# Kernel optimization log

Hardware: AMD Instinct MI355X
Metric: run time of the kernel (lower is better)

Reference implementation:

```python
import jax, jax.numpy as jnp
import numpy as np

INPUT_DIM = 512
LATENT_DIM = 64
H1, H2 = 128, 64  # hardcoded hidden widths in Encoder/Decoder
BATCH = 4096


def _xavier(key, shape):
    fan_out, fan_in = shape
    std = jnp.sqrt(2.0 / (fan_in + fan_out))
    return std * jax.random.normal(key, shape, dtype=jnp.float32)


def setup_inputs() -> dict:
    key = jax.random.key(0)
    ks = jax.random.split(key, 10)
    d = LATENT_DIM
    n_pairs = d * (d - 1) // 2
    n_funcs = 1 + d + n_pairs  # bias + states + pairwise products
    inp = {
        "x": jax.random.normal(ks[0], (BATCH, INPUT_DIM), dtype=jnp.float32),
        "xdot": jax.random.normal(ks[1], (BATCH, INPUT_DIM), dtype=jnp.float32),
        # encoder weights (torch Linear layout: [out, in])
        "We1": _xavier(ks[2], (H1, INPUT_DIM)), "be1": jnp.zeros((H1,), jnp.float32),
        "We2": _xavier(ks[3], (H2, H1)),        "be2": jnp.zeros((H2,), jnp.float32),
        "We3": _xavier(ks[4], (d, H2)),         "be3": jnp.zeros((d,), jnp.float32),
        # decoder weights
        "Wd1": _xavier(ks[5], (H2, d)),         "bd1": jnp.zeros((H2,), jnp.float32),
        "Wd2": _xavier(ks[6], (H1, H2)),        "bd2": jnp.zeros((H1,), jnp.float32),
        "Wd3": _xavier(ks[7], (INPUT_DIM, H1)), "bd3": jnp.zeros((INPUT_DIM,), jnp.float32),
        "XI": jnp.ones((n_funcs, d), jnp.float32),
        "XI_mask": jnp.ones((n_funcs, d), jnp.float32),
    }
    return inp


def _mlp_with_jacobian(x, Ws, bs):
    """3-layer relu MLP; returns output and per-sample analytic Jacobian [B,out,in].
    Jacobian = diag(m3) W3 diag(m2) W2 diag(m1) W1 with relu masks m_l."""
    h = x
    J = None
    for W, b in zip(Ws, bs):
        h = h @ W.T + b                      # [B, out_l]
        m = (h > 0).astype(h.dtype)          # relu mask (grad 0 at 0, matching torch)
        h = jnp.maximum(h, 0)
        Wm = m[:, :, None] * W[None]         # [B, out_l, in_l]
        J = Wm if J is None else jnp.einsum('boh,bhi->boi', Wm, J)
    return h, J


def _sindy_library(z):
    B, d = z.shape
    iu, ju = np.triu_indices(d, k=1)
    ones = jnp.ones((B, 1), z.dtype)
    pairs = z[:, iu] * z[:, ju]              # [B, d(d-1)/2]
    return jnp.concatenate([ones, z, pairs], axis=1)


def reference(x, xdot, We1, be1, We2, be2, We3, be3,
              Wd1, bd1, Wd2, bd2, Wd3, bd3, XI, XI_mask):
    z, Jenc = _mlp_with_jacobian(x, (We1, We2, We3), (be1, be2, be3))
    dz_dt = jnp.einsum('bli,bi->bl', Jenc, xdot)
    xh, Jdec = _mlp_with_jacobian(z, (Wd1, Wd2, Wd3), (bd1, bd2, bd3))
    theta = _sindy_library(z)
    dz_dt_sindy = theta @ (XI_mask * XI)
    dxh_dt = jnp.einsum('bol,bl->bo', Jdec, dz_dt_sindy)
    return (xh, dxh_dt, z, dz_dt, dz_dt_sindy)
```

## Files before the change

### kernel.cpp

```cpp
#include <hip/hip_runtime.h>

#define BATCH 4096
#define IN_DIM 512
#define H1DIM 128
#define H2DIM 64
#define DDIM 64
#define NFUNC 2081
#define NFPAD 2112
#define CHUNK 704
#define KS_PER_CHUNK 22

typedef short bf16x8 __attribute__((ext_vector_type(8)));
typedef float f32x4 __attribute__((ext_vector_type(4)));
#define MFMA(a,b,c) __builtin_amdgcn_mfma_f32_16x16x32_bf16(a,b,c,0,0,0)

#define WSZ1 (H1DIM*IN_DIM)
#define WSZ2 (H2DIM*H1DIM)
#define WSZ3 (DDIM*H2DIM)
#define WSZ4 (H2DIM*DDIM)
#define WSZ5 (H1DIM*H2DIM)
#define WSZ6 (IN_DIM*H1DIM)

__device__ __forceinline__ short f2b(float f) {
    union { float f; unsigned u; } x; x.f = f;
    unsigned r = x.u + 0x7fffu + ((x.u >> 16) & 1u);
    return (short)(r >> 16);
}
__device__ __forceinline__ float b2f(short s) {
    union { unsigned u; float f; } x; x.u = ((unsigned)(unsigned short)s) << 16;
    return x.f;
}
__device__ __forceinline__ void split3f(float v, short& s0, short& s1, short& s2) {
    s0 = f2b(v); float r = v - b2f(s0);
    s1 = f2b(r); float r2 = r - b2f(s1);
    s2 = f2b(r2);
}
__device__ __forceinline__ uint2 pk4(const short* s) {
    union { short s[4]; uint2 u; } z;
    z.s[0] = s[0]; z.s[1] = s[1]; z.s[2] = s[2]; z.s[3] = s[3];
    return z.u;
}

__device__ __forceinline__ void st_b16(short* t, int RS, int r, int c, short v) {
    int b = (c * 2) ^ ((r & 7) << 4);
    *(short*)((char*)(t + r * RS) + b) = v;
}
__device__ __forceinline__ void st_b64(short* t, int RS, int r, int c0, uint2 v) {
    int b = (c0 * 2) ^ ((r & 7) << 4);
    *(uint2*)((char*)(t + r * RS) + b) = v;
}
__device__ __forceinline__ bf16x8 ld_af(const short* t, int RS, int lane, int kbase) {
    int r = lane & 15;
    int b = ((kbase + (lane >> 4) * 8) * 2) ^ ((r & 7) << 4);
    return *(const bf16x8*)((const char*)(t + r * RS) + b);
}
__device__ __forceinline__ bf16x8 ld_bp(const short* P, int blk, int lane) {
    return *(const bf16x8*)(P + ((size_t)blk * 64 + lane) * 8);
}

__device__ __forceinline__ void mf9(bf16x8 f0, bf16x8 f1, bf16x8 f2, bf16x8 fv,
                                    bf16x8 b0, bf16x8 b1, bf16x8 b2,
                                    f32x4& P, f32x4& Q, f32x4& V) {
    P = MFMA(f0, b0, P); Q = MFMA(f1, b1, Q);
    P = MFMA(f1, b0, P); Q = MFMA(f0, b1, Q);
    P = MFMA(f2, b0, P); Q = MFMA(f2, b1, Q);
    P = MFMA(f0, b2, P); Q = MFMA(f1, b2, Q);
    V = MFMA(fv, b0, V);
}

__device__ __forceinline__ void epi_store(short* t0, short* t1, short* t2, short* tv, int RS,
                                          int lane, int col, const f32x4& P, const f32x4& Q,
                                          const f32x4& V, float bb)
{
    #pragma unroll
    for (int q = 0; q < 4; ++q) {
        int row = (lane >> 4) * 4 + q;
        float pre = P[q] + Q[q] + bb;
        float h = fmaxf(pre, 0.f);
        short s0, s1, s2;
        split3f(h, s0, s1, s2);
        st_b16(t0, RS, row, col, s0);
        st_b16(t1, RS, row, col, s1);
        st_b16(t2, RS, row, col, s2);
        st_b16(tv, RS, row, col, pre > 0.f ? f2b(V[q]) : (short)0);
    }
}

template<int K>
__device__ void pack_w(const float* __restrict__ W, short* __restrict__ dst, int NK,
                       int gid, int nthr)
{
    for (int i = gid; i < NK; i += nthr) {
        int c = i / K, k = i % K;
        int cb = c >> 4, ks = k >> 5;
        int L = (((k >> 3) & 3) << 4) | (c & 15);
        int j = k & 7;
        int idx = ((cb * (K / 32) + ks) * 64 + L) * 8 + j;
        short s0, s1, s2; split3f(W[i], s0, s1, s2);
        dst[idx] = s0; dst[idx + NK] = s1; dst[idx + 2 * NK] = s2;
    }
}

__global__ void initk(const float* __restrict__ x, const float* __restrict__ xdot,
                      const float* __restrict__ We1, const float* __restrict__ We2,
                      const float* __restrict__ We3, const float* __restrict__ Wd1,
                      const float* __restrict__ Wd2, const float* __restrict__ Wd3,
                      const float* __restrict__ XI, const float* __restrict__ XIm,
                      float* __restrict__ xh, float* __restrict__ dxh,
                      short* Wp1, short* Wp2, short* Wp3, short* Wp4, short* Wp5, short* Wp6,
                      short* xiP, int2* pk)
{
    int gid = blockIdx.x * blockDim.x + threadIdx.x;
    int nthr = gridDim.x * blockDim.x;

    for (int i = gid; i < (BATCH / 16) * 16 * 64; i += nthr) {
        int L = i & 63, ks = (i >> 6) & 15, rb = i >> 10;
        int row = rb * 16 + (L & 15);
        int k0 = ks * 32 + ((L >> 4) << 3);
        const float* px = &x[(size_t)row * IN_DIM + k0];
        const float* pd = &xdot[(size_t)row * IN_DIM + k0];
        union { short s[8]; bf16x8 v; } a0, a1, a2, dv;
        #pragma unroll
        for (int j = 0; j < 8; ++j) {
            split3f(px[j], a0.s[j], a1.s[j], a2.s[j]);
            dv.s[j] = f2b(pd[j]);
        }
        short* bx = (short*)(xh + (size_t)rb * 8192);
        short* bd = (short*)(dxh + (size_t)rb * 8192);
        int off = (ks * 64 + L) * 8;
        *(bf16x8*)(bx + off) = a0.v;
        *(bf16x8*)(bx + 8192 + off) = a1.v;
        *(bf16x8*)(bd + off) = a2.v;
        *(bf16x8*)(bd + 8192 + off) = dv.v;
    }

    pack_w<512>(We1, Wp1, WSZ1, gid, nthr);
    pack_w<128>(We2, Wp2, WSZ2, gid, nthr);
    pack_w<64>(We3, Wp3, WSZ3, gid, nthr);
    pack_w<64>(Wd1, Wp4, WSZ4, gid, nthr);
    pack_w<64>(Wd2, Wp5, WSZ5, gid, nthr);
    pack_w<128>(Wd3, Wp6, WSZ6, gid, nthr);

    for (int i = gid; i < 4 * 66 * 64; i += nthr) {
        int cb = i / (66 * 64);
        int r = i - cb * (66 * 64);
        int ks = r >> 6, L = r & 63;
        int col = cb * 16 + (L & 15);
        union { short s[8]; bf16x8 v; } w;
        #pragma unroll
        for (int j = 0; j < 8; ++j) {
            int f = ks * 32 + ((L >> 4) << 3) + j;
            float v = (f < NFUNC) ? XI[(size_t)f * DDIM + col] * XIm[(size_t)f * DDIM + col] : 0.f;
            w.s[j] = f2b(v);
        }
        *(bf16x8*)(xiP + (size_t)i * 8) = w.v;
    }

    for (int f = gid; f < NFPAD; f += nthr) {
        int a, b;
        if (f == 0) { a = 64; b = 64; }
        else if (f <= DDIM) { a = f - 1; b = 64; }
        else if (f < NFUNC) {
            int p = f - 1 - DDIM; int i2 = 0, cum = 0;
            while (cum + (63 - i2) <= p) { cum += 63 - i2; ++i2; }
            a = i2; b = i2 + 1 + (p - cum);
        } else { a = 65; b = 65; }
        pk[f] = make_int2(a, b);
    }
}

__global__ __launch_bounds__(256, 1)
void fused(const float* __restrict__ be1, const float* __restrict__ be2,
           const float* __restrict__ be3, const float* __restrict__ bd1,
           const float* __restrict__ bd2, const float* __restrict__ bd3,
           const short* __restrict__ Wp1, const short* __restrict__ Wp2,
           const short* __restrict__ Wp3, const short* __restrict__ Wp4,
           const short* __restrict__ Wp5, const short* __restrict__ Wp6,
           const short* __restrict__ xiP, const int2* __restrict__ pk,
           float* __restrict__ xh, float* __restrict__ dxh, float* __restrict__ zo,
           float* __restrict__ dz, float* __restrict__ dzs)
{
    __shared__ __align__(16) char ldsbuf[37120];
    short* h1s0 = (short*)(ldsbuf + 0);
    short* h1s1 = (short*)(ldsbuf + 4096);
    short* h1s2 = (short*)(ldsbuf + 8192);
    short* v1   = (short*)(ldsbuf + 12288);
    short* h2s0 = (short*)(ldsbuf + 16384);
    short* h2s1 = (short*)(ldsbuf + 18432);
    short* h2s2 = (short*)(ldsbuf + 20480);
    short* v2   = (short*)(ldsbuf + 22528);
    short* th   = (short*)(ldsbuf + 0);
    short* g1s0 = (short*)(ldsbuf + 0);
    short* g1s1 = (short*)(ldsbuf + 2048);
    short* g1s2 = (short*)(ldsbuf + 4096);
    short* u1   = (short*)(ldsbuf + 6144);
    short* g2s0 = (short*)(ldsbuf + 8192);
    short* g2s1 = (short*)(ldsbuf + 12288);
    short* g2s2 = (short*)(ldsbuf + 16384);
    short* u2   = (short*)(ldsbuf + 20480);
    short* zb0  = (short*)(ldsbuf + 24576);
    short* zb1  = (short*)(ldsbuf + 26624);
    short* zb2  = (short*)(ldsbuf + 28672);
    short* dzsb = (short*)(ldsbuf + 30720);
    float* zf   = (float*)(ldsbuf + 32768);

    const int tid = threadIdx.x, lane = tid & 63, wave = tid >> 6;
    const int row0 = blockIdx.x * 16;
    const int c16 = lane & 15;

    float bb1[2] = { be1[wave * 32 + c16], be1[wave * 32 + 16 + c16] };
    float bb2 = be2[wave * 16 + c16];
    float bb3 = be3[wave * 16 + c16];
    float bD1 = bd1[wave * 16 + c16];
    float bD2[2] = { bd2[wave * 32 + c16], bd2[wave * 32 + 16 + c16] };
    float bD3[8];
    #pragma unroll
    for (int i = 0; i < 8; ++i) bD3[i] = bd3[wave * 128 + i * 16 + c16];

    bf16x8 L2B[4][3];

    {
        const short* bx = (const short*)(xh + (size_t)blockIdx.x * 8192);
        const short* bd = (const short*)(dxh + (size_t)blockIdx.x * 8192);
        f32x4 P[2] = {}, Q[2] = {}, V[2] = {};
        bf16x8 A0[3], A1[3], A2[3], Ad[3];
        bf16x8 B0[3][2], B1[3][2], B2[3][2];
#define L1_LA(ks, sl) { int off = ((ks) * 64 + lane) * 8; \
        A0[sl] = *(const bf16x8*)(bx + off); A1[sl] = *(const bf16x8*)(bx + 8192 + off); \
        A2[sl] = *(const bf16x8*)(bd + off); Ad[sl] = *(const bf16x8*)(bd + 8192 + off); }
#define L1_LB(ks, sl) { int bA = (wave * 2) * 16 + (ks), bB = (wave * 2 + 1) * 16 + (ks); \
        B0[sl][0] = ld_bp(Wp1, bA, lane); B1[sl][0] = ld_bp(Wp1 + WSZ1, bA, lane); B2[sl][0] = ld_bp(Wp1 + 2 * WSZ1, bA, lane); \
        B0[sl][1] = ld_bp(Wp1, bB, lane); B1[sl][1] = ld_bp(Wp1 + WSZ1, bB, lane); B2[sl][1] = ld_bp(Wp1 + 2 * WSZ1, bB, lane); }
        L1_LA(0, 0) L1_LB(0, 0)
        L1_LA(1, 1) L1_LB(1, 1)
        L1_LA(2, 2) L1_LB(2, 2)
        #pragma unroll
        for (int ks = 0; ks < 16; ++ks) {
            const int sl = ks % 3;
            mf9(A0[sl], A1[sl], A2[sl], Ad[sl], B0[sl][0], B1[sl][0], B2[sl][0], P[0], Q[0], V[0]);
            mf9(A0[sl], A1[sl], A2[sl], Ad[sl], B0[sl][1], B1[sl][1], B2[sl][1], P[1], Q[1], V[1]);
            if (ks + 3 < 16) { L1_LA(ks + 3, sl) L1_LB(ks + 3, sl) }
        }
#undef L1_LA
#undef L1_LB
        #pragma unroll
        for (int nf = 0; nf < 2; ++nf) {
            int col = wave * 32 + nf * 16 + c16;
            epi_store(h1s0, h1s1, h1s2, v1, 128, lane, col, P[nf], Q[nf], V[nf], bb1[nf]);
        }
        #pragma unroll
        for (int ks = 0; ks < 4; ++ks) {
            int blk = wave * 4 + ks;
            L2B[ks][0] = ld_bp(Wp2, blk, lane);
            L2B[ks][1] = ld_bp(Wp2 + WSZ2, blk, lane);
            L2B[ks][2] = ld_bp(Wp2 + 2 * WSZ2, blk, lane);
        }
    }
    __syncthreads();

    bf16x8 L3B[2][3];
    {
        bf16x8 Aa[4][4];
        #pragma unroll
        for (int ks = 0; ks < 4; ++ks) {
            Aa[ks][0] = ld_af(h1s0, 128, lane, ks * 32);
            Aa[ks][1] = ld_af(h1s1, 128, lane, ks * 32);
            Aa[ks][2] = ld_af(h1s2, 128, lane, ks * 32);
            Aa[ks][3] = ld_af(v1, 128, lane, ks * 32);
        }
        f32x4 P = {}, Q = {}, V = {};
        #pragma unroll
        for (int ks = 0; ks < 4; ++ks)
            mf9(Aa[ks][0], Aa[ks][1], Aa[ks][2], Aa[ks][3], L2B[ks][0], L2B[ks][1], L2B[ks][2], P, Q, V);
        epi_store(h2s0, h2s1, h2s2, v2, 64, lane, wave * 16 + c16, P, Q, V, bb2);
        #pragma unroll
        for (int ks = 0; ks < 2; ++ks) {
            int blk = wave * 2 + ks;
            L3B[ks][0] = ld_bp(Wp3, blk, lane);
            L3B[ks][1] = ld_bp(Wp3 + WSZ3, blk, lane);
            L3B[ks][2] = ld_bp(Wp3 + 2 * WSZ3, blk, lane);
        }
    }
    __syncthreads();

    {
        bf16x8 Aa[2][4];
        #pragma unroll
        for (int ks = 0; ks < 2; ++ks) {
            Aa[ks][0] = ld_af(h2s0, 64, lane, ks * 32);
            Aa[ks][1] = ld_af(h2s1, 64, lane, ks * 32);
            Aa[ks][2] = ld_af(h2s2, 64, lane, ks * 32);
            Aa[ks][3] = ld_af(v2, 64, lane, ks * 32);
        }
        f32x4 P = {}, Q = {}, V = {};
        #pragma unroll
        for (int ks = 0; ks < 2; ++ks)
            mf9(Aa[ks][0], Aa[ks][1], Aa[ks][2], Aa[ks][3], L3B[ks][0], L3B[ks][1], L3B[ks][2], P, Q, V);
        int col = wave * 16 + c16;
        #pragma unroll
        for (int q = 0; q < 4; ++q) {
            int row = (lane >> 4) * 4 + q;
            float pre = P[q] + Q[q] + bb3;
            float hz = fmaxf(pre, 0.f);
            float vz = pre > 0.f ? V[q] : 0.f;
            zf[row * 68 + col] = hz;
            short s0, s1, s2;
            split3f(hz, s0, s1, s2);
            st_b16(zb0, 64, row, col, s0);
            st_b16(zb1, 64, row, col, s1);
            st_b16(zb2, 64, row, col, s2);
            zo[(size_t)(row0 + row) * DDIM + col] = hz;
            dz[(size_t)(row0 + row) * DDIM + col] = vz;
        }
        if (tid < 32) { int r = tid & 15; zf[r * 68 + 64 + (tid >> 4)] = (tid >> 4) ? 0.f : 1.f; }
    }
    __syncthreads();

    {
        f32x4 sa0 = {}, sa1 = {};
        const int tr = tid & 15, tf44 = (tid >> 4) * 44;
        bf16x8 X[KS_PER_CHUNK];
        #pragma unroll
        for (int kk = 0; kk < KS_PER_CHUNK; ++kk)
            X[kk] = ld_bp(xiP, wave * 66 + kk, lane);
        #pragma unroll
        for (int ch = 0; ch < 3; ++ch) {
            #pragma unroll
            for (int g = 0; g < 11; ++g) {
                int fl = tf44 + g * 4;
                int fg = ch * CHUNK + fl;
                int4 qa = *(const int4*)&pk[fg];
                int4 qb = *(const int4*)&pk[fg + 2];
                float t0 = zf[tr * 68 + qa.x] * zf[tr * 68 + qa.y];
                float t1 = zf[tr * 68 + qa.z] * zf[tr * 68 + qa.w];
                float t2 = zf[tr * 68 + qb.x] * zf[tr * 68 + qb.y];
                float t3 = zf[tr * 68 + qb.z] * zf[tr * 68 + qb.w];
                short arr[4] = { f2b(t0), f2b(t1), f2b(t2), f2b(t3) };
                st_b64(th, 704, tr, fl, pk4(arr));
            }
            __syncthreads();
            #pragma unroll
            for (int kk = 0; kk < KS_PER_CHUNK; ++kk) {
                bf16x8 a = ld_af(th, 704, lane, kk * 32);
                if (kk & 1) sa1 = MFMA(a, X[kk], sa1);
                else        sa0 = MFMA(a, X[kk], sa0);
            }
            if (ch < 2) {
                #pragma unroll
                for (int kk = 0; kk < KS_PER_CHUNK; ++kk)
                    X[kk] = ld_bp(xiP, wave * 66 + (ch + 1) * KS_PER_CHUNK + kk, lane);
            }
            __syncthreads();
        }
        f32x4 sacc = sa0 + sa1;
        int col = wave * 16 + c16;
        #pragma unroll
        for (int q = 0; q < 4; ++q) {
            int row = (lane >> 4) * 4 + q;
            float v = sacc[q];
            dzs[(size_t)(row0 + row) * DDIM + col] = v;
            st_b16(dzsb, 64, row, col, f2b(v));
        }
    }
    bf16x8 D1B[2][3];
    #pragma unroll
    for (int ks = 0; ks < 2; ++ks) {
        int blk = wave * 2 + ks;
        D1B[ks][0] = ld_bp(Wp4, blk, lane);
        D1B[ks][1] = ld_bp(Wp4 + WSZ4, blk, lane);
        D1B[ks][2] = ld_bp(Wp4 + 2 * WSZ4, blk, lane);
    }
    __syncthreads();

    bf16x8 D2B[2][2][3];
    {
        bf16x8 Aa[2][4];
        #pragma unroll
        for (int ks = 0; ks < 2; ++ks) {
            Aa[ks][0] = ld_af(zb0, 64, lane, ks * 32);
            Aa[ks][1] = ld_af(zb1, 64, lane, ks * 32);
            Aa[ks][2] = ld_af(zb2, 64, lane, ks * 32);
            Aa[ks][3] = ld_af(dzsb, 64, lane, ks * 32);
        }
        f32x4 P = {}, Q = {}, V = {};
        #pragma unroll
        for (int ks = 0; ks < 2; ++ks)
            mf9(Aa[ks][0], Aa[ks][1], Aa[ks][2], Aa[ks][3], D1B[ks][0], D1B[ks][1], D1B[ks][2], P, Q, V);
        epi_store(g1s0, g1s1, g1s2, u1, 64, lane, wave * 16 + c16, P, Q, V, bD1);
        #pragma unroll
        for (int cf = 0; cf < 2; ++cf)
            #pragma unroll
            for (int ks = 0; ks < 2; ++ks) {
                int blk = (wave * 2 + cf) * 2 + ks;
                D2B[cf][ks][0] = ld_bp(Wp5, blk, lane);
                D2B[cf][ks][1] = ld_bp(Wp5 + WSZ5, blk, lane);
                D2B[cf][ks][2] = ld_bp(Wp5 + 2 * WSZ5, blk, lane);
            }
    }
    __syncthreads();

    {
        bf16x8 Aa[2][4];
        #pragma unroll
        for (int ks = 0; ks < 2; ++ks) {
            Aa[ks][0] = ld_af(g1s0, 64, lane, ks * 32);
            Aa[ks][1] = ld_af(g1s1, 64, lane, ks * 32);
            Aa[ks][2] = ld_af(g1s2, 64, lane, ks * 32);
            Aa[ks][3] = ld_af(u1, 64, lane, ks * 32);
        }
        f32x4 P[2] = {}, Q[2] = {}, V[2] = {};
        #pragma unroll
        for (int cf = 0; cf < 2; ++cf)
            #pragma unroll
            for (int ks = 0; ks < 2; ++ks)
                mf9(Aa[ks][0], Aa[ks][1], Aa[ks][2], Aa[ks][3],
                    D2B[cf][ks][0], D2B[cf][ks][1], D2B[cf][ks][2], P[cf], Q[cf], V[cf]);
        #pragma unroll
        for (int cf = 0; cf < 2; ++cf) {
            int col = wave * 32 + cf * 16 + c16;
            epi_store(g2s0, g2s1, g2s2, u2, 128, lane, col, P[cf], Q[cf], V[cf], bD2[cf]);
        }
    }
    __syncthreads();

    #pragma unroll
    for (int h = 0; h < 2; ++h) {
        f32x4 P[4] = {}, Q[4] = {}, V[4] = {};
        bf16x8 Bp[4][3];
        bf16x8 Ax0[2], Ax1[2], Ax2[2], Axv[2];
#define D3_LA(ks, b) { Ax0[b] = ld_af(g2s0, 128, lane, (ks) * 32); Ax1[b] = ld_af(g2s1, 128, lane, (ks) * 32); \
                       Ax2[b] = ld_af(g2s2, 128, lane, (ks) * 32); Axv[b] = ld_af(u2, 128, lane, (ks) * 32); }
#define D3_LB(s, sl) { int blk = (wave * 8 + h * 4 + ((s) & 3)) * 4 + ((s) >> 2); \
        Bp[sl][0] = ld_bp(Wp6, blk, lane); Bp[sl][1] = ld_bp(Wp6 + WSZ6, blk, lane); Bp[sl][2] = ld_bp(Wp6 + 2 * WSZ6, blk, lane); }
        D3_LA(0, 0)
        D3_LB(0, 0) D3_LB(1, 1) D3_LB(2, 2) D3_LB(3, 3)
        #pragma unroll
        for (int ks = 0; ks < 4; ++ks) {
            if (ks < 3) D3_LA(ks + 1, (ks + 1) & 1)
            #pragma unroll
            for (int cf = 0; cf < 4; ++cf) {
                const int s = ks * 4 + cf, sl = s & 3;
                mf9(Ax0[ks & 1], Ax1[ks & 1], Ax2[ks & 1], Axv[ks & 1],
                    Bp[sl][0], Bp[sl][1], Bp[sl][2], P[cf], Q[cf], V[cf]);
                if (s + 4 < 16) D3_LB(s + 4, sl)
            }
        }
#undef D3_LA
#undef D3_LB
        #pragma unroll
        for (int cf = 0; cf < 4; ++cf) {
            int col = wave * 128 + h * 64 + cf * 16 + c16;
            float bb = bD3[h * 4 + cf];
            #pragma unroll
            for (int q = 0; q < 4; ++q) {
                int row = (lane >> 4) * 4 + q;
                float pre = P[cf][q] + Q[cf][q] + bb;
                xh[(size_t)(row0 + row) * IN_DIM + col] = fmaxf(pre, 0.f);
                dxh[(size_t)(row0 + row) * IN_DIM + col] = pre > 0.f ? V[cf][q] : 0.f;
            }
        }
    }
}

extern "C" void kernel_launch(void* const* d_in, const int* in_sizes, int n_in,
                              void* d_out, int out_size, void* d_ws, size_t ws_size,
                              hipStream_t stream)
{
    const float* x    = (const float*)d_in[0];
    const float* xdot = (const float*)d_in[1];
    const float* We1  = (const float*)d_in[2];
    const float* be1  = (const float*)d_in[3];
    const float* We2  = (const float*)d_in[4];
    const float* be2  = (const float*)d_in[5];
    const float* We3  = (const float*)d_in[6];
    const float* be3  = (const float*)d_in[7];
    const float* Wd1  = (const float*)d_in[8];
    const float* bd1  = (const float*)d_in[9];
    const float* Wd2  = (const float*)d_in[10];
    const float* bd2  = (const float*)d_in[11];
    const float* Wd3  = (const float*)d_in[12];
    const float* bd3  = (const float*)d_in[13];
    const float* XI   = (const float*)d_in[14];
    const float* XIm  = (const float*)d_in[15];

    float* out = (float*)d_out;
    float* xh  = out;
    float* dxh = out + (size_t)BATCH * IN_DIM;
    float* zo  = dxh + (size_t)BATCH * IN_DIM;
    float* dz  = zo + (size_t)BATCH * DDIM;
    float* dzs = dz + (size_t)BATCH * DDIM;

    int2*  pk  = (int2*)d_ws;
    short* Wp1 = (short*)(pk + NFPAD);
    short* Wp2 = Wp1 + 3 * WSZ1;
    short* Wp3 = Wp2 + 3 * WSZ2;
    short* Wp4 = Wp3 + 3 * WSZ3;
    short* Wp5 = Wp4 + 3 * WSZ4;
    short* Wp6 = Wp5 + 3 * WSZ5;
    short* xiP = Wp6 + 3 * WSZ6;

    initk<<<1024, 256, 0, stream>>>(x, xdot, We1, We2, We3, Wd1, Wd2, Wd3, XI, XIm,
                                    xh, dxh, Wp1, Wp2, Wp3, Wp4, Wp5, Wp6, xiP, pk);
    fused<<<BATCH / 16, 256, 0, stream>>>(be1, be2, be3, bd1, bd2, bd3,
                                          Wp1, Wp2, Wp3, Wp4, Wp5, Wp6, xiP, pk,
                                          xh, dxh, zo, dz, dzs);
}
```

Before: 51.31 us.

## Stream layer-1 and decoder-3 operands through LDS with async global_load_lds pipeline

Replaces the register-prefetched global loads in the first encoder GEMM and the last decoder GEMM with asynchronous global-to-LDS copies (global_load_lds) into per-wave multi-slot ring buffers. Explicit vmcnt waits and sched barriers control how far the loads run ahead. Several weight prefetches (Wp2, Wp3, XI, Wp4, Wp5) are also moved earlier so they overlap preceding MFMA work. LDS grows to 120KB, which keeps occupancy at one block per CU, and the hand-tuned waitcnt values are fragile if the instruction count changes.

```diff
diff --git a/kernel.cpp b/kernel.cpp
--- a/kernel.cpp
+++ b/kernel.cpp
@@ -39,6 +39,11 @@
     union { short s[4]; uint2 u; } z;
     z.s[0] = s[0]; z.s[1] = s[1]; z.s[2] = s[2]; z.s[3] = s[3];
     return z.u;
+}
+
+template<int N> __device__ __forceinline__ void waitv() {
+    asm volatile("s_waitcnt vmcnt(%0)" :: "n"(N) : "memory");
+    __builtin_amdgcn_sched_barrier(0);
 }
 
 __device__ __forceinline__ void st_b16(short* t, int RS, int r, int c, short v) {
@@ -180,33 +185,39 @@
            float* __restrict__ xh, float* __restrict__ dxh, float* __restrict__ zo,
            float* __restrict__ dz, float* __restrict__ dzs)
 {
-    __shared__ __align__(16) char ldsbuf[37120];
-    short* h1s0 = (short*)(ldsbuf + 0);
-    short* h1s1 = (short*)(ldsbuf + 4096);
-    short* h1s2 = (short*)(ldsbuf + 8192);
-    short* v1   = (short*)(ldsbuf + 12288);
-    short* h2s0 = (short*)(ldsbuf + 16384);
-    short* h2s1 = (short*)(ldsbuf + 18432);
-    short* h2s2 = (short*)(ldsbuf + 20480);
-    short* v2   = (short*)(ldsbuf + 22528);
-    short* th   = (short*)(ldsbuf + 0);
-    short* g1s0 = (short*)(ldsbuf + 0);
-    short* g1s1 = (short*)(ldsbuf + 2048);
-    short* g1s2 = (short*)(ldsbuf + 4096);
-    short* u1   = (short*)(ldsbuf + 6144);
-    short* g2s0 = (short*)(ldsbuf + 8192);
-    short* g2s1 = (short*)(ldsbuf + 12288);
-    short* g2s2 = (short*)(ldsbuf + 16384);
-    short* u2   = (short*)(ldsbuf + 20480);
-    short* zb0  = (short*)(ldsbuf + 24576);
-    short* zb1  = (short*)(ldsbuf + 26624);
-    short* zb2  = (short*)(ldsbuf + 28672);
-    short* dzsb = (short*)(ldsbuf + 30720);
-    float* zf   = (float*)(ldsbuf + 32768);
+    __shared__ __align__(1024) char lds[122880];
+#define GLL(gp, lo) __builtin_amdgcn_global_load_lds( \
+        (const __attribute__((address_space(1))) unsigned int*)(gp), \
+        (__attribute__((address_space(3))) unsigned int*)&lds[lo], 16, 0, 0)
+
+    short* h1s0 = (short*)(lds + 0);
+    short* h1s1 = (short*)(lds + 4096);
+    short* h1s2 = (short*)(lds + 8192);
+    short* v1   = (short*)(lds + 12288);
+    short* h2s0 = (short*)(lds + 16384);
+    short* h2s1 = (short*)(lds + 18432);
+    short* h2s2 = (short*)(lds + 20480);
+    short* v2   = (short*)(lds + 22528);
+    short* th   = (short*)(lds + 0);
+    short* g1s0 = (short*)(lds + 0);
+    short* g1s1 = (short*)(lds + 2048);
+    short* g1s2 = (short*)(lds + 4096);
+    short* u1   = (short*)(lds + 6144);
+    short* g2s0 = (short*)(lds + 8192);
+    short* g2s1 = (short*)(lds + 12288);
+    short* g2s2 = (short*)(lds + 16384);
+    short* u2   = (short*)(lds + 20480);
+    short* zb0  = (short*)(lds + 24576);
+    short* zb1  = (short*)(lds + 26624);
+    short* zb2  = (short*)(lds + 28672);
+    short* dzsb = (short*)(lds + 30720);
+    float* zf   = (float*)(lds + 32768);
 
     const int tid = threadIdx.x, lane = tid & 63, wave = tid >> 6;
     const int row0 = blockIdx.x * 16;
     const int c16 = lane & 15;
+    const int lane16 = lane * 16;
+    const int tr = tid & 15, tf44 = (tid >> 4) * 44;
 
     float bb1[2] = { be1[wave * 32 + c16], be1[wave * 32 + 16 + c16] };
     float bb2 = be2[wave * 16 + c16];
@@ -217,44 +228,61 @@
     #pragma unroll
     for (int i = 0; i < 8; ++i) bD3[i] = bd3[wave * 128 + i * 16 + c16];
 
+    f32x4 P1[2] = {}, Q1[2] = {}, V1[2] = {};
+    {
+        const char* bxc = (const char*)(xh + (size_t)blockIdx.x * 8192);
+        const char* bdc = (const char*)(dxh + (size_t)blockIdx.x * 8192);
+        const char* w1ac = (const char*)Wp1;
+        const char* w1bc = (const char*)(Wp1 + WSZ1);
+        const char* w1cc = (const char*)(Wp1 + 2 * WSZ1);
+#define SLOT1(d) (unsigned)(wave * 30720 + (d) * 10240)
+#define ISS1(ks, d) { unsigned sb = SLOT1(d); \
+        const char* ga = bxc + (ks) * 1024 + lane16; \
+        GLL(ga, sb);            GLL(ga + 16384, sb + 1024); \
+        const char* gd = bdc + (ks) * 1024 + lane16; \
+        GLL(gd, sb + 2048);     GLL(gd + 16384, sb + 3072); \
+        int bA = ((wave * 2) * 16 + (ks)) * 1024 + lane16; \
+        int bB = ((wave * 2 + 1) * 16 + (ks)) * 1024 + lane16; \
+        GLL(w1ac + bA, sb + 4096); GLL(w1bc + bA, sb + 5120); GLL(w1cc + bA, sb + 6144); \
+        GLL(w1ac + bB, sb + 7168); GLL(w1bc + bB, sb + 8192); GLL(w1cc + bB, sb + 9216); }
+#define STEP1(ks, WN) { waitv<WN>(); unsigned sb = SLOT1((ks) % 3); \
+        bf16x8 f0  = *(const bf16x8*)&lds[sb + lane16]; \
+        bf16x8 f1  = *(const bf16x8*)&lds[sb + 1024 + lane16]; \
+        bf16x8 f2  = *(const bf16x8*)&lds[sb + 2048 + lane16]; \
+        bf16x8 fv  = *(const bf16x8*)&lds[sb + 3072 + lane16]; \
+        bf16x8 b00 = *(const bf16x8*)&lds[sb + 4096 + lane16]; \
+        bf16x8 b01 = *(const bf16x8*)&lds[sb + 5120 + lane16]; \
+        bf16x8 b02 = *(const bf16x8*)&lds[sb + 6144 + lane16]; \
+        bf16x8 b10 = *(const bf16x8*)&lds[sb + 7168 + lane16]; \
+        bf16x8 b11 = *(const bf16x8*)&lds[sb + 8192 + lane16]; \
+        bf16x8 b12 = *(const bf16x8*)&lds[sb + 9216 + lane16]; \
+        mf9(f0, f1, f2, fv, b00, b01, b02, P1[0], Q1[0], V1[0]); \
+        mf9(f0, f1, f2, fv, b10, b11, b12, P1[1], Q1[1], V1[1]); \
+        __builtin_amdgcn_sched_barrier(0); \
+        if ((ks) + 3 < 16) ISS1((ks) + 3, (ks) % 3) }
+
+        ISS1(0, 0) ISS1(1, 1) ISS1(2, 2)
+        STEP1(0, 20)  STEP1(1, 20)  STEP1(2, 20)  STEP1(3, 20)
+        STEP1(4, 20)  STEP1(5, 20)  STEP1(6, 20)  STEP1(7, 20)
+        STEP1(8, 20)  STEP1(9, 20)  STEP1(10, 20) STEP1(11, 20)
+        STEP1(12, 20) STEP1(13, 20) STEP1(14, 10) STEP1(15, 0)
+#undef ISS1
+#undef STEP1
+#undef SLOT1
+    }
+    __syncthreads();
+    #pragma unroll
+    for (int nf = 0; nf < 2; ++nf) {
+        int col = wave * 32 + nf * 16 + c16;
+        epi_store(h1s0, h1s1, h1s2, v1, 128, lane, col, P1[nf], Q1[nf], V1[nf], bb1[nf]);
+    }
     bf16x8 L2B[4][3];
-
-    {
-        const short* bx = (const short*)(xh + (size_t)blockIdx.x * 8192);
-        const short* bd = (const short*)(dxh + (size_t)blockIdx.x * 8192);
-        f32x4 P[2] = {}, Q[2] = {}, V[2] = {};
-        bf16x8 A0[3], A1[3], A2[3], Ad[3];
-        bf16x8 B0[3][2], B1[3][2], B2[3][2];
-#define L1_LA(ks, sl) { int off = ((ks) * 64 + lane) * 8; \
-        A0[sl] = *(const bf16x8*)(bx + off); A1[sl] = *(const bf16x8*)(bx + 8192 + off); \
-        A2[sl] = *(const bf16x8*)(bd + off); Ad[sl] = *(const bf16x8*)(bd + 8192 + off); }
-#define L1_LB(ks, sl) { int bA = (wave * 2) * 16 + (ks), bB = (wave * 2 + 1) * 16 + (ks); \
-        B0[sl][0] = ld_bp(Wp1, bA, lane); B1[sl][0] = ld_bp(Wp1 + WSZ1, bA, lane); B2[sl][0] = ld_bp(Wp1 + 2 * WSZ1, bA, lane); \
-        B0[sl][1] = ld_bp(Wp1, bB, lane); B1[sl][1] = ld_bp(Wp1 + WSZ1, bB, lane); B2[sl][1] = ld_bp(Wp1 + 2 * WSZ1, bB, lane); }
-        L1_LA(0, 0) L1_LB(0, 0)
-        L1_LA(1, 1) L1_LB(1, 1)
-        L1_LA(2, 2) L1_LB(2, 2)
-        #pragma unroll
-        for (int ks = 0; ks < 16; ++ks) {
-            const int sl = ks % 3;
-            mf9(A0[sl], A1[sl], A2[sl], Ad[sl], B0[sl][0], B1[sl][0], B2[sl][0], P[0], Q[0], V[0]);
-            mf9(A0[sl], A1[sl], A2[sl], Ad[sl], B0[sl][1], B1[sl][1], B2[sl][1], P[1], Q[1], V[1]);
-            if (ks + 3 < 16) { L1_LA(ks + 3, sl) L1_LB(ks + 3, sl) }
-        }
-#undef L1_LA
-#undef L1_LB
-        #pragma unroll
-        for (int nf = 0; nf < 2; ++nf) {
-            int col = wave * 32 + nf * 16 + c16;
-            epi_store(h1s0, h1s1, h1s2, v1, 128, lane, col, P[nf], Q[nf], V[nf], bb1[nf]);
-        }
-        #pragma unroll
-        for (int ks = 0; ks < 4; ++ks) {
-            int blk = wave * 4 + ks;
-            L2B[ks][0] = ld_bp(Wp2, blk, lane);
-            L2B[ks][1] = ld_bp(Wp2 + WSZ2, blk, lane);
-            L2B[ks][2] = ld_bp(Wp2 + 2 * WSZ2, blk, lane);
-        }
+    #pragma unroll
+    for (int ks = 0; ks < 4; ++ks) {
+        int blk = wave * 4 + ks;
+        L2B[ks][0] = ld_bp(Wp2, blk, lane);
+        L2B[ks][1] = ld_bp(Wp2 + WSZ2, blk, lane);
+        L2B[ks][2] = ld_bp(Wp2 + 2 * WSZ2, blk, lane);
     }
     __syncthreads();
 
@@ -268,11 +296,6 @@
             Aa[ks][2] = ld_af(h1s2, 128, lane, ks * 32);
             Aa[ks][3] = ld_af(v1, 128, lane, ks * 32);
         }
-        f32x4 P = {}, Q = {}, V = {};
-        #pragma unroll
-        for (int ks = 0; ks < 4; ++ks)
-            mf9(Aa[ks][0], Aa[ks][1], Aa[ks][2], Aa[ks][3], L2B[ks][0], L2B[ks][1], L2B[ks][2], P, Q, V);
-        epi_store(h2s0, h2s1, h2s2, v2, 64, lane, wave * 16 + c16, P, Q, V, bb2);
         #pragma unroll
         for (int ks = 0; ks < 2; ++ks) {
             int blk = wave * 2 + ks;
@@ -280,9 +303,15 @@
             L3B[ks][1] = ld_bp(Wp3 + WSZ3, blk, lane);
             L3B[ks][2] = ld_bp(Wp3 + 2 * WSZ3, blk, lane);
         }
-    }
-    __syncthreads();
-
+        f32x4 P = {}, Q = {}, V = {};
+        #pragma unroll
+        for (int ks = 0; ks < 4; ++ks)
+            mf9(Aa[ks][0], Aa[ks][1], Aa[ks][2], Aa[ks][3], L2B[ks][0], L2B[ks][1], L2B[ks][2], P, Q, V);
+        epi_store(h2s0, h2s1, h2s2, v2, 64, lane, wave * 16 + c16, P, Q, V, bb2);
+    }
+    __syncthreads();
+
+    bf16x8 X[KS_PER_CHUNK];
     {
         bf16x8 Aa[2][4];
         #pragma unroll
@@ -296,6 +325,9 @@
         #pragma unroll
         for (int ks = 0; ks < 2; ++ks)
             mf9(Aa[ks][0], Aa[ks][1], Aa[ks][2], Aa[ks][3], L3B[ks][0], L3B[ks][1], L3B[ks][2], P, Q, V);
+        #pragma unroll
+        for (int kk = 0; kk < KS_PER_CHUNK; ++kk)
+            X[kk] = ld_bp(xiP, wave * 66 + kk, lane);
         int col = wave * 16 + c16;
         #pragma unroll
         for (int q = 0; q < 4; ++q) {
@@ -316,43 +348,46 @@
     }
     __syncthreads();
 
-    {
-        f32x4 sa0 = {}, sa1 = {};
-        const int tr = tid & 15, tf44 = (tid >> 4) * 44;
-        bf16x8 X[KS_PER_CHUNK];
-        #pragma unroll
-        for (int kk = 0; kk < KS_PER_CHUNK; ++kk)
-            X[kk] = ld_bp(xiP, wave * 66 + kk, lane);
-        #pragma unroll
-        for (int ch = 0; ch < 3; ++ch) {
-            #pragma unroll
-            for (int g = 0; g < 11; ++g) {
-                int fl = tf44 + g * 4;
-                int fg = ch * CHUNK + fl;
-                int4 qa = *(const int4*)&pk[fg];
-                int4 qb = *(const int4*)&pk[fg + 2];
-                float t0 = zf[tr * 68 + qa.x] * zf[tr * 68 + qa.y];
-                float t1 = zf[tr * 68 + qa.z] * zf[tr * 68 + qa.w];
-                float t2 = zf[tr * 68 + qb.x] * zf[tr * 68 + qb.y];
-                float t3 = zf[tr * 68 + qb.z] * zf[tr * 68 + qb.w];
-                short arr[4] = { f2b(t0), f2b(t1), f2b(t2), f2b(t3) };
-                st_b64(th, 704, tr, fl, pk4(arr));
-            }
-            __syncthreads();
-            #pragma unroll
-            for (int kk = 0; kk < KS_PER_CHUNK; ++kk) {
-                bf16x8 a = ld_af(th, 704, lane, kk * 32);
-                if (kk & 1) sa1 = MFMA(a, X[kk], sa1);
-                else        sa0 = MFMA(a, X[kk], sa0);
-            }
-            if (ch < 2) {
-                #pragma unroll
-                for (int kk = 0; kk < KS_PER_CHUNK; ++kk)
-                    X[kk] = ld_bp(xiP, wave * 66 + (ch + 1) * KS_PER_CHUNK + kk, lane);
-            }
-            __syncthreads();
-        }
+    f32x4 sa0 = {}, sa1 = {};
+#define BUILD(ch) { _Pragma("unroll") for (int g = 0; g < 11; ++g) { \
+        int fl = tf44 + g * 4, fg = (ch) * CHUNK + fl; \
+        int4 qa = *(const int4*)&pk[fg]; int4 qb = *(const int4*)&pk[fg + 2]; \
+        float t0 = zf[tr * 68 + qa.x] * zf[tr * 68 + qa.y]; \
+        float t1 = zf[tr * 68 + qa.z] * zf[tr * 68 + qa.w]; \
+        float t2 = zf[tr * 68 + qb.x] * zf[tr * 68 + qb.y]; \
+        float t3 = zf[tr * 68 + qb.z] * zf[tr * 68 + qb.w]; \
+        short arr[4] = { f2b(t0), f2b(t1), f2b(t2), f2b(t3) }; \
+        st_b64(th, 704, tr, fl, pk4(arr)); } }
+#define SMF() { _Pragma("unroll") for (int kk = 0; kk < KS_PER_CHUNK; ++kk) { \
+        bf16x8 a = ld_af(th, 704, lane, kk * 32); \
+        if (kk & 1) sa1 = MFMA(a, X[kk], sa1); else sa0 = MFMA(a, X[kk], sa0); } }
+#define ISX(ch) { _Pragma("unroll") for (int kk = 0; kk < KS_PER_CHUNK; ++kk) \
+        X[kk] = ld_bp(xiP, wave * 66 + (ch) * KS_PER_CHUNK + kk, lane); }
+
+    BUILD(0)
+    __syncthreads();
+    SMF() ISX(1)
+    __syncthreads();
+    BUILD(1)
+    __syncthreads();
+    SMF() ISX(2)
+    __syncthreads();
+    BUILD(2)
+    __syncthreads();
+    SMF()
+#undef BUILD
+#undef SMF
+#undef ISX
+    bf16x8 D1B[2][3];
+    {
         f32x4 sacc = sa0 + sa1;
+        #pragma unroll
+        for (int ks = 0; ks < 2; ++ks) {
+            int blk = wave * 2 + ks;
+            D1B[ks][0] = ld_bp(Wp4, blk, lane);
+            D1B[ks][1] = ld_bp(Wp4 + WSZ4, blk, lane);
+            D1B[ks][2] = ld_bp(Wp4 + 2 * WSZ4, blk, lane);
+        }
         int col = wave * 16 + c16;
         #pragma unroll
         for (int q = 0; q < 4; ++q) {
@@ -362,17 +397,9 @@
             st_b16(dzsb, 64, row, col, f2b(v));
         }
     }
-    bf16x8 D1B[2][3];
-    #pragma unroll
-    for (int ks = 0; ks < 2; ++ks) {
-        int blk = wave * 2 + ks;
-        D1B[ks][0] = ld_bp(Wp4, blk, lane);
-        D1B[ks][1] = ld_bp(Wp4 + WSZ4, blk, lane);
-        D1B[ks][2] = ld_bp(Wp4 + 2 * WSZ4, blk, lane);
-    }
-    __syncthreads();
-
-    bf16x8 D2B[2][2][3];
+    __syncthreads();
+
+    bf16x8 D2B[4][3];
     {
         bf16x8 Aa[2][4];
         #pragma unroll
@@ -382,20 +409,20 @@
             Aa[ks][2] = ld_af(zb2, 64, lane, ks * 32);
             Aa[ks][3] = ld_af(dzsb, 64, lane, ks * 32);
         }
-        f32x4 P = {}, Q = {}, V = {};
-        #pragma unroll
-        for (int ks = 0; ks < 2; ++ks)
-            mf9(Aa[ks][0], Aa[ks][1], Aa[ks][2], Aa[ks][3], D1B[ks][0], D1B[ks][1], D1B[ks][2], P, Q, V);
-        epi_store(g1s0, g1s1, g1s2, u1, 64, lane, wave * 16 + c16, P, Q, V, bD1);
         #pragma unroll
         for (int cf = 0; cf < 2; ++cf)
             #pragma unroll
             for (int ks = 0; ks < 2; ++ks) {
                 int blk = (wave * 2 + cf) * 2 + ks;
-                D2B[cf][ks][0] = ld_bp(Wp5, blk, lane);
-                D2B[cf][ks][1] = ld_bp(Wp5 + WSZ5, blk, lane);
-                D2B[cf][ks][2] = ld_bp(Wp5 + 2 * WSZ5, blk, lane);
+                D2B[cf * 2 + ks][0] = ld_bp(Wp5, blk, lane);
+                D2B[cf * 2 + ks][1] = ld_bp(Wp5 + WSZ5, blk, lane);
+                D2B[cf * 2 + ks][2] = ld_bp(Wp5 + 2 * WSZ5, blk, lane);
             }
+        f32x4 P = {}, Q = {}, V = {};
+        #pragma unroll
+        for (int ks = 0; ks < 2; ++ks)
+            mf9(Aa[ks][0], Aa[ks][1], Aa[ks][2], Aa[ks][3], D1B[ks][0], D1B[ks][1], D1B[ks][2], P, Q, V);
+        epi_store(g1s0, g1s1, g1s2, u1, 64, lane, wave * 16 + c16, P, Q, V, bD1);
     }
     __syncthreads();
 
@@ -414,7 +441,8 @@
             #pragma unroll
             for (int ks = 0; ks < 2; ++ks)
                 mf9(Aa[ks][0], Aa[ks][1], Aa[ks][2], Aa[ks][3],
-                    D2B[cf][ks][0], D2B[cf][ks][1], D2B[cf][ks][2], P[cf], Q[cf], V[cf]);
+                    D2B[cf * 2 + ks][0], D2B[cf * 2 + ks][1], D2B[cf * 2 + ks][2],
+                    P[cf], Q[cf], V[cf]);
         #pragma unroll
         for (int cf = 0; cf < 2; ++cf) {
             int col = wave * 32 + cf * 16 + c16;
@@ -423,43 +451,57 @@
     }
     __syncthreads();
 
-    #pragma unroll
-    for (int h = 0; h < 2; ++h) {
+    bf16x8 Ax0, Ax1, Ax2, Axv;
+    const char* w6ac = (const char*)Wp6;
+    const char* w6bc = (const char*)(Wp6 + WSZ6);
+    const char* w6cc = (const char*)(Wp6 + 2 * WSZ6);
+#define D3SLOT(d) (unsigned)(40960 + wave * 12288 + (d) * 3072)
+#define D3ISS(h, s) { unsigned sb = D3SLOT((s) & 3); \
+        int bo = ((wave * 8 + (h) * 4 + ((s) & 3)) * 4 + ((s) >> 2)) * 1024 + lane16; \
+        GLL(w6ac + bo, sb); GLL(w6bc + bo, sb + 1024); GLL(w6cc + bo, sb + 2048); }
+#define D3STEP(h, s, WN, Pa, Qa, Va) { waitv<WN>(); \
+        if (((s) & 3) == 0) { int ks = (s) >> 2; \
+            Ax0 = ld_af(g2s0, 128, lane, ks * 32); Ax1 = ld_af(g2s1, 128, lane, ks * 32); \
+            Ax2 = ld_af(g2s2, 128, lane, ks * 32); Axv = ld_af(u2, 128, lane, ks * 32); } \
+        { unsigned sb = D3SLOT((s) & 3); \
+          bf16x8 c0 = *(const bf16x8*)&lds[sb + lane16]; \
+          bf16x8 c1 = *(const bf16x8*)&lds[sb + 1024 + lane16]; \
+          bf16x8 c2 = *(const bf16x8*)&lds[sb + 2048 + lane16]; \
+          mf9(Ax0, Ax1, Ax2, Axv, c0, c1, c2, Pa[(s) & 3], Qa[(s) & 3], Va[(s) & 3]); } \
+        __builtin_amdgcn_sched_barrier(0); \
+        if ((s) + 4 < 16) D3ISS(h, (s) + 4) }
+#define D3EPI(h, P_, Q_, V_) { _Pragma("unroll") for (int cf = 0; cf < 4; ++cf) { \
+        int col = wave * 128 + (h) * 64 + cf * 16 + c16; \
+        float bb = bD3[(h) * 4 + cf]; \
+        _Pragma("unroll") for (int q = 0; q < 4; ++q) { \
+            int row = (lane >> 4) * 4 + q; \
+            float pre = P_[cf][q] + Q_[cf][q] + bb; \
+            xh[(size_t)(row0 + row) * IN_DIM + col] = fmaxf(pre, 0.f); \
+            dxh[(size_t)(row0 + row) * IN_DIM + col] = pre > 0.f ? V_[cf][q] : 0.f; } } }
+
+    {
         f32x4 P[4] = {}, Q[4] = {}, V[4] = {};
-        bf16x8 Bp[4][3];
-        bf16x8 Ax0[2], Ax1[2], Ax2[2], Axv[2];
-#define D3_LA(ks, b) { Ax0[b] = ld_af(g2s0, 128, lane, (ks) * 32); Ax1[b] = ld_af(g2s1, 128, lane, (ks) * 32); \
-                       Ax2[b] = ld_af(g2s2, 128, lane, (ks) * 32); Axv[b] = ld_af(u2, 128, lane, (ks) * 32); }
-#define D3_LB(s, sl) { int blk = (wave * 8 + h * 4 + ((s) & 3)) * 4 + ((s) >> 2); \
-        Bp[sl][0] = ld_bp(Wp6, blk, lane); Bp[sl][1] = ld_bp(Wp6 + WSZ6, blk, lane); Bp[sl][2] = ld_bp(Wp6 + 2 * WSZ6, blk, lane); }
-        D3_LA(0, 0)
-        D3_LB(0, 0) D3_LB(1, 1) D3_LB(2, 2) D3_LB(3, 3)
-        #pragma unroll
-        for (int ks = 0; ks < 4; ++ks) {
-            if (ks < 3) D3_LA(ks + 1, (ks + 1) & 1)
-            #pragma unroll
-            for (int cf = 0; cf < 4; ++cf) {
-                const int s = ks * 4 + cf, sl = s & 3;
-                mf9(Ax0[ks & 1], Ax1[ks & 1], Ax2[ks & 1], Axv[ks & 1],
-                    Bp[sl][0], Bp[sl][1], Bp[sl][2], P[cf], Q[cf], V[cf]);
-                if (s + 4 < 16) D3_LB(s + 4, sl)
-            }
-        }
-#undef D3_LA
-#undef D3_LB
-        #pragma unroll
-        for (int cf = 0; cf < 4; ++cf) {
-            int col = wave * 128 + h * 64 + cf * 16 + c16;
-            float bb = bD3[h * 4 + cf];
-            #pragma unroll
-            for (int q = 0; q < 4; ++q) {
-                int row = (lane >> 4) * 4 + q;
-                float pre = P[cf][q] + Q[cf][q] + bb;
-                xh[(size_t)(row0 + row) * IN_DIM + col] = fmaxf(pre, 0.f);
-                dxh[(size_t)(row0 + row) * IN_DIM + col] = pre > 0.f ? V[cf][q] : 0.f;
-            }
-        }
-    }
+        D3ISS(0, 0) D3ISS(0, 1) D3ISS(0, 2) D3ISS(0, 3)
+        D3STEP(0, 0, 9, P, Q, V)  D3STEP(0, 1, 9, P, Q, V)  D3STEP(0, 2, 9, P, Q, V)  D3STEP(0, 3, 9, P, Q, V)
+        D3STEP(0, 4, 9, P, Q, V)  D3STEP(0, 5, 9, P, Q, V)  D3STEP(0, 6, 9, P, Q, V)  D3STEP(0, 7, 9, P, Q, V)
+        D3STEP(0, 8, 9, P, Q, V)  D3STEP(0, 9, 9, P, Q, V)  D3STEP(0, 10, 9, P, Q, V) D3STEP(0, 11, 9, P, Q, V)
+        D3STEP(0, 12, 9, P, Q, V) D3STEP(0, 13, 6, P, Q, V) D3STEP(0, 14, 3, P, Q, V) D3STEP(0, 15, 0, P, Q, V)
+        D3EPI(0, P, Q, V)
+    }
+    {
+        f32x4 P[4] = {}, Q[4] = {}, V[4] = {};
+        D3ISS(1, 0) D3ISS(1, 1) D3ISS(1, 2) D3ISS(1, 3)
+        D3STEP(1, 0, 9, P, Q, V)  D3STEP(1, 1, 9, P, Q, V)  D3STEP(1, 2, 9, P, Q, V)  D3STEP(1, 3, 9, P, Q, V)
+        D3STEP(1, 4, 9, P, Q, V)  D3STEP(1, 5, 9, P, Q, V)  D3STEP(1, 6, 9, P, Q, V)  D3STEP(1, 7, 9, P, Q, V)
+        D3STEP(1, 8, 9, P, Q, V)  D3STEP(1, 9, 9, P, Q, V)  D3STEP(1, 10, 9, P, Q, V) D3STEP(1, 11, 9, P, Q, V)
+        D3STEP(1, 12, 9, P, Q, V) D3STEP(1, 13, 6, P, Q, V) D3STEP(1, 14, 3, P, Q, V) D3STEP(1, 15, 0, P, Q, V)
+        D3EPI(1, P, Q, V)
+    }
+#undef D3ISS
+#undef D3STEP
+#undef D3EPI
+#undef D3SLOT
+#undef GLL
 }
 
 extern "C" void kernel_launch(void* const* d_in, const int* in_sizes, int n_in,
```

After: 48.65 us. 5.2% less time.
